# Performance work log

Hardware: AMD Instinct MI355X
Metric: run time of the kernel (lower is better)

The kernel has to match this reference:

```python
import jax, jax.numpy as jnp
import numpy as np

# Bone edge list (0-indexed) from _calc_length_single, in original order.
_BONES = np.array([
    (3, 2), (2, 20), (20, 8), (8, 9), (9, 10), (10, 11),
    (20, 4), (4, 5), (5, 6), (6, 7),
    (20, 1), (1, 0), (0, 16), (16, 17), (17, 18), (18, 19),
    (0, 12), (12, 13), (13, 14), (14, 15),
], dtype=np.int32)
_A = jnp.asarray(_BONES[:, 0])
_B = jnp.asarray(_BONES[:, 1])


def _bone_lengths(joints):
    # joints: [B, 21, 3] -> [B, 20]
    diff = joints[:, _A, :] - joints[:, _B, :]
    return jnp.linalg.norm(diff, axis=-1)


def setup_inputs() -> dict:
    key = jax.random.key(0)
    k1, k2 = jax.random.split(key)
    B = 524288
    pred_joints = jax.random.normal(k1, (B, 21, 3), dtype=jnp.float32)
    gt_joints = jax.random.normal(k2, (B, 21, 3), dtype=jnp.float32)
    return {"pred_joints": pred_joints, "gt_joints": gt_joints}


def reference(pred_joints, gt_joints):
    pred_len = _bone_lengths(pred_joints)   # [B, 20]
    gt_len = _bone_lengths(gt_joints)       # [B, 20]
    rel = jnp.abs(pred_len - gt_len) / gt_len
    # mean over 20 bones per sample, then mean over batch == global mean
    return jnp.mean(rel)
```

## Files before the change

kernel.cpp:

```cpp
#include <hip/hip_runtime.h>
#include <hip/hip_bf16.h>


#define TILE_BYTES   16128
#define TILE_PAD_F   4096
#define NBLOCKS      512

static constexpr int BA[20] = {3,2,20,8,9,10,20,4,5,6,20,1,0,16,17,18,0,12,13,14};
static constexpr int BB[20] = {2,20,8,9,10,11,4,5,6,7,1,0,16,17,18,19,12,13,14,15};

typedef __attribute__((address_space(1))) const void gvoid_t;
typedef __attribute__((address_space(3))) void lvoid_t;

__global__ __launch_bounds__(256)
void jll_kernel(const float* __restrict__ pred,
                const float* __restrict__ gt,
                float* __restrict__ partials,
                int tiles_per_block) {
    __shared__ __align__(16) float lds[2][2][TILE_PAD_F];
    __shared__ float wsum[4];

    const int tid  = threadIdx.x;
    const int wave = tid >> 6;
    const int lane = tid & 63;

    const int g = tid & 3;
    int ja[5], jb[5];
    #pragma unroll
    for (int k = 0; k < 5; ++k) {
        ja[k] = 3 * ((g == 0) ? BA[k] : (g == 1) ? BA[5 + k] : (g == 2) ? BA[10 + k] : BA[15 + k]);
        jb[k] = 3 * ((g == 0) ? BB[k] : (g == 1) ? BB[5 + k] : (g == 2) ? BB[10 + k] : BB[15 + k]);
    }
    const int smoff = (tid >> 2) * 63;

    const size_t tile0 = (size_t)blockIdx.x * tiles_per_block;

    auto STAGE = [&](int q, size_t tile) {
        const char* srcP = (const char*)pred + tile * (size_t)TILE_BYTES;
        const char* srcG = (const char*)gt   + tile * (size_t)TILE_BYTES;
        #pragma unroll
        for (int c = 0; c < 4; ++c) {
            const int chunk = wave * 4 + c;
            int off = chunk * 1024 + lane * 16;
            if (off > TILE_BYTES - 16) off = TILE_BYTES - 16;
            __builtin_amdgcn_global_load_lds(
                (gvoid_t*)(srcP + off), (lvoid_t*)&lds[q][0][chunk * 256], 16, 0, 0);
            __builtin_amdgcn_global_load_lds(
                (gvoid_t*)(srcG + off), (lvoid_t*)&lds[q][1][chunk * 256], 16, 0, 0);
        }
    };

    float sum = 0.0f;

    STAGE(0, tile0);

    for (int t = 0; t < tiles_per_block; ++t) {
        if (t + 1 < tiles_per_block) {
            STAGE((t + 1) & 1, tile0 + t + 1);
            asm volatile("s_waitcnt vmcnt(8)\n\ts_barrier" ::: "memory");
        } else {
            asm volatile("s_waitcnt vmcnt(0)\n\ts_barrier" ::: "memory");
        }
        __builtin_amdgcn_sched_barrier(0);

        {
            const float* SP = &lds[t & 1][0][smoff];
            const float* SG = &lds[t & 1][1][smoff];
            #pragma unroll
            for (int k = 0; k < 5; ++k) {
                const int a = ja[k], c = jb[k];
                float dx = SP[a + 0] - SP[c + 0];
                float dy = SP[a + 1] - SP[c + 1];
                float dz = SP[a + 2] - SP[c + 2];
                float pl = sqrtf(dx * dx + dy * dy + dz * dz);
                float ex = SG[a + 0] - SG[c + 0];
                float ey = SG[a + 1] - SG[c + 1];
                float ez = SG[a + 2] - SG[c + 2];
                float gl = sqrtf(ex * ex + ey * ey + ez * ez);
                sum += fabsf(pl - gl) / gl;
            }
        }

        asm volatile("s_waitcnt lgkmcnt(0)\n\ts_barrier" ::: "memory");
    }

    #pragma unroll
    for (int off = 32; off > 0; off >>= 1)
        sum += __shfl_down(sum, off);

    if (lane == 0) wsum[wave] = sum;
    __syncthreads();
    if (tid == 0)
        partials[blockIdx.x] = wsum[0] + wsum[1] + wsum[2] + wsum[3];
}

__global__ __launch_bounds__(256)
void jll_final_kernel(const float* __restrict__ partials, int nparts,
                      float* __restrict__ out, float inv_count) {
    const int tid = threadIdx.x;
    float sum = 0.0f;
    for (int i = tid; i < nparts; i += 256) sum += partials[i];

    #pragma unroll
    for (int off = 32; off > 0; off >>= 1)
        sum += __shfl_down(sum, off);

    __shared__ float wsum[4];
    const int lane = tid & 63;
    const int wid  = tid >> 6;
    if (lane == 0) wsum[wid] = sum;
    __syncthreads();
    if (tid == 0)
        out[0] = (wsum[0] + wsum[1] + wsum[2] + wsum[3]) * inv_count;
}

extern "C" void kernel_launch(void* const* d_in, const int* in_sizes, int n_in,
                              void* d_out, int out_size, void* d_ws, size_t ws_size,
                              hipStream_t stream) {
    const float* pred = (const float*)d_in[0];
    const float* gt   = (const float*)d_in[1];
    float* out = (float*)d_out;
    float* partials = (float*)d_ws;

    const int nsamples = in_sizes[0] / 63;
    const int ntiles   = nsamples / 64;
    const int tiles_per_block = ntiles / NBLOCKS;

    jll_kernel<<<NBLOCKS, 256, 0, stream>>>(pred, gt, partials, tiles_per_block);

    const float inv_count = 1.0f / ((float)nsamples * 20.0f);
    jll_final_kernel<<<1, 256, 0, stream>>>(partials, NBLOCKS, out, inv_count);
}
```

Baseline: 49.56 us.

## Reuse shared joints across bone chains and fuse final reduction via atomicAdd

Each thread's five bones are reordered into a 7-joint chain table so every joint coordinate is read from LDS once into registers, replacing the ten endpoint reads per bone group. The second reduction kernel is removed: each block scales its partial sum and atomically adds it into the output, which is zeroed with a memset first. This cuts LDS reads and one kernel launch. In exchange it adds a memset, and the float atomics make the summation order nondeterministic.

After: 52.58 us. 6.1% more time.

```diff
diff --git a/kernel.cpp b/kernel.cpp
--- a/kernel.cpp
+++ b/kernel.cpp
@@ -6,8 +6,12 @@
 #define TILE_PAD_F   4096
 #define NBLOCKS      512
 
-static constexpr int BA[20] = {3,2,20,8,9,10,20,4,5,6,20,1,0,16,17,18,0,12,13,14};
-static constexpr int BB[20] = {2,20,8,9,10,11,4,5,6,7,1,0,16,17,18,19,12,13,14,15};
+static constexpr int JT0[7] = {3,2,2,20,8,9,10};
+static constexpr int JT1[7] = {10,11,20,4,5,6,7};
+static constexpr int JT2[7] = {20,1,1,0,16,17,18};
+static constexpr int JT3[7] = {18,19,0,12,13,14,15};
+static constexpr int EA[5] = {0,2,3,4,5};
+static constexpr int EB[5] = {1,3,4,5,6};
 
 typedef __attribute__((address_space(1))) const void gvoid_t;
 typedef __attribute__((address_space(3))) void lvoid_t;
@@ -15,7 +19,8 @@
 __global__ __launch_bounds__(256)
 void jll_kernel(const float* __restrict__ pred,
                 const float* __restrict__ gt,
-                float* __restrict__ partials,
+                float* __restrict__ out,
+                float inv_count,
                 int tiles_per_block) {
     __shared__ __align__(16) float lds[2][2][TILE_PAD_F];
     __shared__ float wsum[4];
@@ -25,11 +30,10 @@
     const int lane = tid & 63;
 
     const int g = tid & 3;
-    int ja[5], jb[5];
+    int JT[7];
     #pragma unroll
-    for (int k = 0; k < 5; ++k) {
-        ja[k] = 3 * ((g == 0) ? BA[k] : (g == 1) ? BA[5 + k] : (g == 2) ? BA[10 + k] : BA[15 + k]);
-        jb[k] = 3 * ((g == 0) ? BB[k] : (g == 1) ? BB[5 + k] : (g == 2) ? BB[10 + k] : BB[15 + k]);
+    for (int k = 0; k < 7; ++k) {
+        JT[k] = 3 * ((g == 0) ? JT0[k] : (g == 1) ? JT1[k] : (g == 2) ? JT2[k] : JT3[k]);
     }
     const int smoff = (tid >> 2) * 63;
 
@@ -66,16 +70,23 @@
         {
             const float* SP = &lds[t & 1][0][smoff];
             const float* SG = &lds[t & 1][1][smoff];
+            float px[7], py[7], pz[7], qx[7], qy[7], qz[7];
             #pragma unroll
-            for (int k = 0; k < 5; ++k) {
-                const int a = ja[k], c = jb[k];
-                float dx = SP[a + 0] - SP[c + 0];
-                float dy = SP[a + 1] - SP[c + 1];
-                float dz = SP[a + 2] - SP[c + 2];
+            for (int k = 0; k < 7; ++k) {
+                const int o = JT[k];
+                px[k] = SP[o + 0]; py[k] = SP[o + 1]; pz[k] = SP[o + 2];
+                qx[k] = SG[o + 0]; qy[k] = SG[o + 1]; qz[k] = SG[o + 2];
+            }
+            #pragma unroll
+            for (int e = 0; e < 5; ++e) {
+                const int a = EA[e], b = EB[e];
+                float dx = px[a] - px[b];
+                float dy = py[a] - py[b];
+                float dz = pz[a] - pz[b];
                 float pl = sqrtf(dx * dx + dy * dy + dz * dz);
-                float ex = SG[a + 0] - SG[c + 0];
-                float ey = SG[a + 1] - SG[c + 1];
-                float ez = SG[a + 2] - SG[c + 2];
+                float ex = qx[a] - qx[b];
+                float ey = qy[a] - qy[b];
+                float ez = qz[a] - qz[b];
                 float gl = sqrtf(ex * ex + ey * ey + ez * ez);
                 sum += fabsf(pl - gl) / gl;
             }
@@ -91,27 +102,7 @@
     if (lane == 0) wsum[wave] = sum;
     __syncthreads();
     if (tid == 0)
-        partials[blockIdx.x] = wsum[0] + wsum[1] + wsum[2] + wsum[3];
-}
-
-__global__ __launch_bounds__(256)
-void jll_final_kernel(const float* __restrict__ partials, int nparts,
-                      float* __restrict__ out, float inv_count) {
-    const int tid = threadIdx.x;
-    float sum = 0.0f;
-    for (int i = tid; i < nparts; i += 256) sum += partials[i];
-
-    #pragma unroll
-    for (int off = 32; off > 0; off >>= 1)
-        sum += __shfl_down(sum, off);
-
-    __shared__ float wsum[4];
-    const int lane = tid & 63;
-    const int wid  = tid >> 6;
-    if (lane == 0) wsum[wid] = sum;
-    __syncthreads();
-    if (tid == 0)
-        out[0] = (wsum[0] + wsum[1] + wsum[2] + wsum[3]) * inv_count;
+        atomicAdd(out, (wsum[0] + wsum[1] + wsum[2] + wsum[3]) * inv_count);
 }
 
 extern "C" void kernel_launch(void* const* d_in, const int* in_sizes, int n_in,
@@ -120,14 +111,14 @@
     const float* pred = (const float*)d_in[0];
     const float* gt   = (const float*)d_in[1];
     float* out = (float*)d_out;
-    float* partials = (float*)d_ws;
 
     const int nsamples = in_sizes[0] / 63;
     const int ntiles   = nsamples / 64;
     const int tiles_per_block = ntiles / NBLOCKS;
 
-    jll_kernel<<<NBLOCKS, 256, 0, stream>>>(pred, gt, partials, tiles_per_block);
+    const float inv_count = 1.0f / ((float)nsamples * 20.0f);
 
-    const float inv_count = 1.0f / ((float)nsamples * 20.0f);
-    jll_final_kernel<<<1, 256, 0, stream>>>(partials, NBLOCKS, out, inv_count);
+    hipMemsetAsync(out, 0, sizeof(float), stream);
+
+    jll_kernel<<<NBLOCKS, 256, 0, stream>>>(pred, gt, out, inv_count, tiles_per_block);
 }
```
